# Kernel tuning notes

Hardware: AMD Instinct MI355X
Metric: run time of the kernel (lower is better)

Reference implementation:

```python
import jax, jax.numpy as jnp
import numpy as np

B, L, DIM, H, D = 4, 1024, 1024, 8, 32


def setup_inputs() -> dict:
    key = jax.random.key(0)
    ks = jax.random.split(key, 8)
    s = 0.02
    return dict(
        x=jax.random.normal(ks[0], (B, L, DIM), jnp.float32),
        W_in=jax.random.normal(ks[1], (DIM, DIM), jnp.float32) * s,
        b_in=jnp.zeros((DIM,), jnp.float32),
        W_qkva=jax.random.normal(ks[2], (H * D * 8, DIM), jnp.float32) * s,
        b_qkva=jnp.zeros((H * D * 8,), jnp.float32),
        W_y=jax.random.normal(ks[3], (DIM, H * D * 2), jnp.float32) * s,
        b_y=jnp.zeros((DIM,), jnp.float32),
        W_out=jax.random.normal(ks[4], (DIM, DIM), jnp.float32) * s,
        b_out=jnp.zeros((DIM,), jnp.float32),
        h0_re=jax.random.normal(ks[5], (H, D, D), jnp.float32),
        h0_im=jax.random.normal(ks[6], (H, D, D), jnp.float32),
    )


def reference(x, W_in, b_in, W_qkva, b_qkva, W_y, b_y, W_out, b_out, h0_re, h0_im):
    b, Ls, dim = x.shape
    Hh, Dd = h0_re.shape[0], h0_re.shape[1]
    u = jax.nn.silu(x @ W_in.T + b_in)
    qkva = (u @ W_qkva.T + b_qkva).reshape(b, Ls, Hh, Dd, 4, 2)
    c = jax.lax.complex(qkva[..., 0], qkva[..., 1])  # [b,L,H,D,4] complex
    q, k, v, a = c[..., 0], c[..., 1], c[..., 2], c[..., 3]
    mag2 = a.real * a.real + a.imag * a.imag
    # unit-modulus rotation scaled by sigmoid(log|a|^2) gate
    a = a * (jax.lax.rsqrt(mag2) * jax.nn.sigmoid(jnp.log(mag2)))
    kv = jnp.einsum('blhd,blhe->blhde', k, v)  # [b,L,H,D,D] complex
    h0 = jax.lax.complex(h0_re, h0_im)[None]  # [1,H,D,D]
    # fold initial state into step 0: h_0 = a_0 * h_init + kv_0
    kv = kv.at[:, 0].add(a[:, 0, ..., None] * h0)
    a_e = a[..., None]  # [b,L,H,D,1], broadcasts over state col dim

    def comb(c1, c2):
        a1, x1 = c1
        a2, x2 = c2
        return (a1 * a2, a2 * x1 + x2)

    # linear recurrence h_l = a_l * h_{l-1} + kv_l (equiv. to the FFT/cumsum
    # triangular-product matrix in the original module)
    _, h = jax.lax.associative_scan(comb, (a_e, kv), axis=1)
    y = jnp.einsum('blhd,blhde->blhe', q, h)  # [b,L,H,D] complex
    y2 = jnp.stack([y.real, y.imag], axis=-1).reshape(b, Ls, Hh * Dd * 2)
    y2 = jax.nn.silu(y2 @ W_y.T + b_y)
    return y2 @ W_out.T + b_out
```

## Files before the change

kernel.cpp:

```cpp
#include <hip/hip_runtime.h>

#define B_ 4
#define L_ 1024
#define DIM_ 1024
#define H_ 8
#define D_ 32
#define LSEG 32
#define NSEG (L_/LSEG)

typedef __bf16 bf16_t;
typedef __bf16 bf16x8 __attribute__((ext_vector_type(8)));
typedef float f32x4 __attribute__((ext_vector_type(4)));

__device__ __forceinline__ void gload_lds16(const bf16_t* g, bf16_t* l) {
  __builtin_amdgcn_global_load_lds((const __attribute__((address_space(1))) void*)g,
                                   (__attribute__((address_space(3))) void*)l, 16, 0, 0);
}
__device__ __forceinline__ void gload_lds16f(const float* g, float* l) {
  __builtin_amdgcn_global_load_lds((const __attribute__((address_space(1))) void*)g,
                                   (__attribute__((address_space(3))) void*)l, 16, 0, 0);
}

__global__ __launch_bounds__(256) void cvt_all(const float* __restrict__ x,
                                               const float* __restrict__ w1,
                                               const float* __restrict__ w2,
                                               const float* __restrict__ w3,
                                               const float* __restrict__ w4,
                                               bf16_t* __restrict__ ox,
                                               bf16_t* __restrict__ o1,
                                               bf16_t* __restrict__ o2,
                                               bf16_t* __restrict__ o3,
                                               bf16_t* __restrict__ o4) {
  int g = blockIdx.x;
  const float* in; bf16_t* out; int i;
  if      (g < 4096) { in = x;  out = ox; i = g * 256 + threadIdx.x; }
  else if (g < 5120) { in = w1; out = o1; i = (g - 4096) * 256 + threadIdx.x; }
  else if (g < 7168) { in = w2; out = o2; i = (g - 5120) * 256 + threadIdx.x; }
  else if (g < 7680) { in = w3; out = o3; i = (g - 7168) * 256 + threadIdx.x; }
  else               { in = w4; out = o4; i = (g - 7680) * 256 + threadIdx.x; }
  float4 v = ((const float4*)in)[i];
  union { bf16_t b[4]; unsigned long long q; } pk;
  pk.b[0] = (bf16_t)v.x; pk.b[1] = (bf16_t)v.y;
  pk.b[2] = (bf16_t)v.z; pk.b[3] = (bf16_t)v.w;
  ((unsigned long long*)out)[i] = pk.q;
}

template<int BN, int ACT, int OUTBF, int GATE>
__global__ __launch_bounds__(256) void gemm_nt(const bf16_t* __restrict__ A,
                                               const bf16_t* __restrict__ Bm,
                                               const float* __restrict__ bias,
                                               void* __restrict__ Cout,
                                               int M, int N, int K) {
  constexpr int NI = BN / 32;
  constexpr int ISS_B = BN / 32;
  __shared__ __align__(16) bf16_t As[128 * 64];
  __shared__ __align__(16) bf16_t Bs[BN * 64];
  const int t = threadIdx.x;
  const int wid = t >> 6, lane = t & 63;
  const int wr = wid >> 1, wc = wid & 1;
  const int lr = lane & 15, lq = lane >> 4;
  const int bm = blockIdx.x, bn = blockIdx.y;
  const int rA = wid * 32 + (lane >> 3);
  const int rB = wid * (BN / 4) + (lane >> 3);
  const int c8 = (((lane & 7) ^ ((lane >> 3) & 7))) * 8;
  const bf16_t* Ag = A + (size_t)(bm * 128 + rA) * K + c8;
  const bf16_t* Bg = Bm + (size_t)(bn * BN + rB) * K + c8;
  bf16_t* AsW = As + (wid * 32) * 64;
  bf16_t* BsW = Bs + (wid * (BN / 4)) * 64;
  f32x4 acc[4][NI] = {};
  for (int k0 = 0; k0 < K; k0 += 64) {
#pragma unroll
    for (int j = 0; j < 4; ++j)
      gload_lds16(Ag + (size_t)j * 8 * K, AsW + j * 8 * 64);
#pragma unroll
    for (int j = 0; j < ISS_B; ++j)
      gload_lds16(Bg + (size_t)j * 8 * K, BsW + j * 8 * 64);
    Ag += 64; Bg += 64;
    __syncthreads();
#pragma unroll
    for (int ks = 0; ks < 2; ++ks) {
      const int sg = ks * 4 + lq;
      const int sl = (sg ^ (lr & 7)) * 8;
      bf16x8 af[4], bfv[NI];
#pragma unroll
      for (int mi = 0; mi < 4; ++mi)
        af[mi] = *(const bf16x8*)&As[(wr * 64 + mi * 16 + lr) * 64 + sl];
#pragma unroll
      for (int ni = 0; ni < NI; ++ni)
        bfv[ni] = *(const bf16x8*)&Bs[(wc * (BN/2) + ni * 16 + lr) * 64 + sl];
#pragma unroll
      for (int mi = 0; mi < 4; ++mi)
#pragma unroll
        for (int ni = 0; ni < NI; ++ni)
          acc[mi][ni] = __builtin_amdgcn_mfma_f32_16x16x32_bf16(af[mi], bfv[ni], acc[mi][ni], 0, 0, 0);
    }
    __syncthreads();
  }
#pragma unroll
  for (int mi = 0; mi < 4; ++mi) {
#pragma unroll
    for (int ni = 0; ni < NI; ++ni) {
      int colg = bn * BN + wc * (BN/2) + ni * 16 + lr;
      float bb = bias[colg];
#pragma unroll
      for (int r = 0; r < 4; ++r) {
        int rowg = bm * 128 + wr * 64 + mi * 16 + lq * 4 + r;
        float v = acc[mi][ni][r] + bb;
        if (ACT == 1) v = v / (1.0f + __expf(-v));
        if (GATE) {
          float wv = __shfl_xor(v, 1);
          if ((colg & 7) >= 6) {
            float m2 = v * v + wv * wv;
            v *= sqrtf(m2) / (1.0f + m2);
          }
        }
        if (OUTBF) ((bf16_t*)Cout)[(size_t)rowg * N + colg] = (bf16_t)v;
        else       ((float*)Cout)[(size_t)rowg * N + colg] = v;
      }
    }
  }
}

template<int ACT, int OUTBF>
__global__ __launch_bounds__(256) void gemm64k(const bf16_t* __restrict__ A,
                                               const bf16_t* __restrict__ Bm,
                                               const float* __restrict__ bias,
                                               void* __restrict__ Cout,
                                               int M, int N, int K) {
  __shared__ __align__(16) bf16_t As[64 * 128];
  __shared__ __align__(16) bf16_t Bs[64 * 128];
  const int t = threadIdx.x;
  const int wid = t >> 6, lane = t & 63;
  const int wr = wid >> 1, wc = wid & 1;
  const int lr = lane & 15, lq = lane >> 4;
  const int bm = blockIdx.x, bn = blockIdx.y;
  const int crow = wid * 4 + (lane >> 4);
  const int c8 = ((lane & 15) ^ crow) * 8;
  const bf16_t* Ag = A + (size_t)(bm * 64 + crow) * K + c8;
  const bf16_t* Bg = Bm + (size_t)(bn * 64 + crow) * K + c8;
  bf16_t* AsW = As + (wid * 4) * 128;
  bf16_t* BsW = Bs + (wid * 4) * 128;
  f32x4 acc[2][2] = {};
  for (int k0 = 0; k0 < K; k0 += 128) {
#pragma unroll
    for (int j = 0; j < 4; ++j)
      gload_lds16(Ag + (size_t)j * 16 * K, AsW + j * 16 * 128);
#pragma unroll
    for (int j = 0; j < 4; ++j)
      gload_lds16(Bg + (size_t)j * 16 * K, BsW + j * 16 * 128);
    Ag += 128; Bg += 128;
    __syncthreads();
#pragma unroll
    for (int ks = 0; ks < 4; ++ks) {
      const int sg = ks * 4 + lq;
      const int sl = (sg ^ lr) * 8;
      bf16x8 af[2], bfv[2];
#pragma unroll
      for (int mi = 0; mi < 2; ++mi)
        af[mi] = *(const bf16x8*)&As[(wr * 32 + mi * 16 + lr) * 128 + sl];
#pragma unroll
      for (int ni = 0; ni < 2; ++ni)
        bfv[ni] = *(const bf16x8*)&Bs[(wc * 32 + ni * 16 + lr) * 128 + sl];
#pragma unroll
      for (int mi = 0; mi < 2; ++mi)
#pragma unroll
        for (int ni = 0; ni < 2; ++ni)
          acc[mi][ni] = __builtin_amdgcn_mfma_f32_16x16x32_bf16(af[mi], bfv[ni], acc[mi][ni], 0, 0, 0);
    }
    __syncthreads();
  }
#pragma unroll
  for (int mi = 0; mi < 2; ++mi) {
#pragma unroll
    for (int ni = 0; ni < 2; ++ni) {
      int colg = bn * 64 + wc * 32 + ni * 16 + lr;
      float bb = bias[colg];
#pragma unroll
      for (int r = 0; r < 4; ++r) {
        int rowg = bm * 64 + wr * 32 + mi * 16 + lq * 4 + r;
        float v = acc[mi][ni][r] + bb;
        if (ACT == 1) v = v / (1.0f + __expf(-v));
        if (OUTBF) ((bf16_t*)Cout)[(size_t)rowg * N + colg] = (bf16_t)v;
        else       ((float*)Cout)[(size_t)rowg * N + colg] = v;
      }
    }
  }
}

__global__ __launch_bounds__(256) void scan_seg(const float* __restrict__ qkva,
                                                float* __restrict__ y_loc,
                                                float* __restrict__ qP,
                                                float* __restrict__ Aseg,
                                                float* __restrict__ Hfin) {
  __shared__ __align__(16) float Q[LSEG * 256];
  const int t = threadIdx.x;
  const int seg = blockIdx.x;
  const int s = seg & (NSEG - 1);
  const int bh = seg >> 5;
  const int h = bh & (H_ - 1), b = bh >> 3;
  const int wid = t >> 6, lane = t & 63;
  const int dg = lane & 7, eh = lane >> 3;
  const int e = wid * 8 + eh;
  const float* gb = qkva + ((size_t)(b * L_ + s * LSEG) * H_ + h) * 256;
#pragma unroll
  for (int j = 0; j < 8; ++j) {
    const int l = wid * 8 + j;
    gload_lds16f(gb + (size_t)l * (H_ * 256) + lane * 4, Q + l * 256);
  }
  __syncthreads();
  float hr[4] = {}, hi[4] = {};
  float Pr[4] = {1,1,1,1}, Pi[4] = {0,0,0,0};
  const size_t row0 = ((size_t)(b * L_ + s * LSEG) * H_ + h) * D_;

  float4 qkA[4], qkB[4];
  float2 aaA[4], aaB[4];
  float2 vvA, vvB;

  auto LOADR = [&](int l, float4 (&qk)[4], float2 (&aa)[4], float2& vv) {
    const float* R = Q + l * 256;
    vv = *(const float2*)(R + e * 8 + 4);
#pragma unroll
    for (int j = 0; j < 4; ++j) {
      qk[j] = *(const float4*)(R + (dg + 8 * j) * 8);
      aa[j] = *(const float2*)(R + (dg + 8 * j) * 8 + 6);
    }
  };

  auto STEP = [&](int l, float4 (&qk)[4], float2 (&aa)[4], float2& vv) {
    const size_t rowl = row0 + (size_t)l * (H_ * D_);
    float ytr = 0.f, yti = 0.f;
    if (wid == 0) {
      float2 qpv[4];
#pragma unroll
      for (int j = 0; j < 4; ++j) {
        float nPr = aa[j].x * Pr[j] - aa[j].y * Pi[j];
        float nPi = aa[j].x * Pi[j] + aa[j].y * Pr[j];
        Pr[j] = nPr; Pi[j] = nPi;
        qpv[j].x = qk[j].x * nPr - qk[j].y * nPi;
        qpv[j].y = qk[j].x * nPi + qk[j].y * nPr;
      }
      if (lane < 8) {
#pragma unroll
        for (int j = 0; j < 4; ++j)
          *(float2*)(qP + (rowl + dg + 8 * j) * 2) = qpv[j];
      }
    }
#pragma unroll
    for (int j = 0; j < 4; ++j) {
      float kvr = qk[j].z * vv.x - qk[j].w * vv.y;
      float kvi = qk[j].z * vv.y + qk[j].w * vv.x;
      float nhr = aa[j].x * hr[j] - aa[j].y * hi[j] + kvr;
      float nhi = aa[j].x * hi[j] + aa[j].y * hr[j] + kvi;
      hr[j] = nhr; hi[j] = nhi;
      ytr += qk[j].x * nhr - qk[j].y * nhi;
      yti += qk[j].x * nhi + qk[j].y * nhr;
    }
    ytr += __shfl_down(ytr, 4); yti += __shfl_down(yti, 4);
    ytr += __shfl_down(ytr, 2); yti += __shfl_down(yti, 2);
    ytr += __shfl_down(ytr, 1); yti += __shfl_down(yti, 1);
    if (dg == 0)
      *(float2*)(y_loc + (rowl + e) * 2) = make_float2(ytr, yti);
  };

  LOADR(0, qkA, aaA, vvA);
  for (int l = 0; l < LSEG; l += 2) {
    LOADR(l + 1, qkB, aaB, vvB);
    STEP(l, qkA, aaA, vvA);
    LOADR(l + 2 < LSEG ? l + 2 : LSEG - 1, qkA, aaA, vvA);
    STEP(l + 1, qkB, aaB, vvB);
  }

  const size_t segb = (size_t)seg * D_;
  if (t < 8) {
#pragma unroll
    for (int j = 0; j < 4; ++j)
      *(float2*)(Aseg + (segb + dg + 8 * j) * 2) = make_float2(Pr[j], Pi[j]);
  }
#pragma unroll
  for (int j = 0; j < 4; ++j)
    *(float2*)(Hfin + ((segb + dg + 8 * j) * D_ + e) * 2) = make_float2(hr[j], hi[j]);
}

__global__ __launch_bounds__(128) void seg_combine(const float* __restrict__ h0re,
                                                   const float* __restrict__ h0im,
                                                   const float* __restrict__ Aseg,
                                                   const float* __restrict__ Hfin,
                                                   float* __restrict__ Hc) {
  const int bh = blockIdx.x >> 3;
  const int eg = blockIdx.x & 7;
  const int h = bh & (H_ - 1);
  const int t = threadIdx.x;
  const int d = t >> 2;
  const int e = eg * 4 + (t & 3);
  float cr = h0re[((size_t)h * D_ + d) * D_ + e];
  float ci = h0im[((size_t)h * D_ + d) * D_ + e];
  const size_t idx0  = ((size_t)bh * NSEG * D_ + d) * D_ + e;
  const size_t aidx0 = (size_t)bh * NSEG * D_ + d;
  float2 Ab[8], Fb[8];
#pragma unroll
  for (int p = 0; p < 8; ++p) {
    Ab[p] = *(const float2*)(Aseg + (aidx0 + (size_t)p * D_) * 2);
    Fb[p] = *(const float2*)(Hfin + (idx0 + (size_t)p * D_ * D_) * 2);
  }
  for (int so = 0; so < NSEG; so += 8) {
#pragma unroll
    for (int p = 0; p < 8; ++p) {
      const int s = so + p;
      float2 A0 = Ab[p], F0 = Fb[p];
      if (so + 8 < NSEG) {
        Ab[p] = *(const float2*)(Aseg + (aidx0 + (size_t)(s + 8) * D_) * 2);
        Fb[p] = *(const float2*)(Hfin + (idx0 + (size_t)(s + 8) * D_ * D_) * 2);
      }
      *(float2*)(Hc + (idx0 + (size_t)s * D_ * D_) * 2) = make_float2(cr, ci);
      float nr = A0.x * cr - A0.y * ci + F0.x;
      float ni = A0.x * ci + A0.y * cr + F0.y;
      cr = nr; ci = ni;
    }
  }
}

__global__ __launch_bounds__(256) void y_correct(const float* __restrict__ y_loc,
                                                 const float* __restrict__ qP,
                                                 const float* __restrict__ Hc,
                                                 bf16_t* __restrict__ y2b) {
  __shared__ __align__(16) float Hs[D_ * D_ * 2];
  const int seg = blockIdx.x;
  const int s = seg & (NSEG - 1);
  const int bh = seg >> 5;
  const int h = bh & (H_ - 1), b = bh >> 3;
  const int t = threadIdx.x;
  const float4* src = (const float4*)(Hc + (size_t)seg * (D_ * D_ * 2));
  ((float4*)Hs)[t] = src[t];
  ((float4*)Hs)[t + 256] = src[t + 256];
  __syncthreads();
  const int ep = (t & 15) * 2;
#pragma unroll
  for (int half = 0; half < 2; ++half) {
    const int l = half * 16 + (t >> 4);
    const int lg = s * LSEG + l;
    const size_t rowc = ((size_t)(b * L_ + lg) * H_ + h) * D_;
    const float* qpr = qP + rowc * 2;
    float4 y0 = *(const float4*)(y_loc + (rowc + ep) * 2);
    float ac_r[2] = {y0.x, y0.z}, ac_i[2] = {y0.y, y0.w};
#pragma unroll 4
    for (int d = 0; d < D_; ++d) {
      float2 p = *(const float2*)(qpr + d * 2);
      float4 hv = *(const float4*)&Hs[(d * D_ + ep) * 2];
      ac_r[0] += p.x * hv.x - p.y * hv.y; ac_i[0] += p.x * hv.y + p.y * hv.x;
      ac_r[1] += p.x * hv.z - p.y * hv.w; ac_i[1] += p.x * hv.w + p.y * hv.z;
    }
    union { bf16_t bv[4]; uint2 q; } pk;
    pk.bv[0] = (bf16_t)ac_r[0]; pk.bv[1] = (bf16_t)ac_i[0];
    pk.bv[2] = (bf16_t)ac_r[1]; pk.bv[3] = (bf16_t)ac_i[1];
    *(uint2*)(y2b + (size_t)(b * L_ + lg) * (H_ * D_ * 2) + (h * D_ + ep) * 2) = pk.q;
  }
}

extern "C" void kernel_launch(void* const* d_in, const int* in_sizes, int n_in,
                              void* d_out, int out_size, void* d_ws, size_t ws_size,
                              hipStream_t stream) {
  const float* x      = (const float*)d_in[0];
  const float* W_in   = (const float*)d_in[1];
  const float* b_in   = (const float*)d_in[2];
  const float* W_qkva = (const float*)d_in[3];
  const float* b_qkva = (const float*)d_in[4];
  const float* W_y    = (const float*)d_in[5];
  const float* b_y    = (const float*)d_in[6];
  const float* W_out  = (const float*)d_in[7];
  const float* b_out  = (const float*)d_in[8];
  const float* h0re   = (const float*)d_in[9];
  const float* h0im   = (const float*)d_in[10];

  char* w = (char*)d_ws;
  const size_t MB = 1ull << 20;
  bf16_t* Wb_in   = (bf16_t*)(w + 0*MB);
  bf16_t* Wb_qkva = (bf16_t*)(w + 2*MB);
  bf16_t* Wb_y    = (bf16_t*)(w + 6*MB);
  bf16_t* Wb_out  = (bf16_t*)(w + 7*MB);
  bf16_t* xb      = (bf16_t*)(w + 9*MB);
  float*  qP      = (float*) (w + 9*MB);
  bf16_t* u       = (bf16_t*)(w + 17*MB);
  float*  y_loc   = (float*) (w + 17*MB);
  float*  qkva    = (float*) (w + 25*MB);
  float*  Hc      = (float*) (w + 25*MB);
  bf16_t* y2b     = (bf16_t*)(w + 41*MB);
  bf16_t* z       = (bf16_t*)(w + 45*MB);
  float*  Aseg    = (float*) (w + 57*MB);
  float*  Hfin    = (float*) (w + 58*MB);

  cvt_all<<<8704, 256, 0, stream>>>(x, W_in, W_qkva, W_y, W_out,
                                    xb, Wb_in, Wb_qkva, Wb_y, Wb_out);

  gemm64k<1,1><<<dim3(64, 16), 256, 0, stream>>>(xb, Wb_in, b_in, u, 4096, 1024, 1024);
  gemm_nt<64,0,0,1><<<dim3(32, 32), 256, 0, stream>>>(u, Wb_qkva, b_qkva, qkva, 4096, 2048, 1024);
  scan_seg   <<<1024, 256, 0, stream>>>(qkva, y_loc, qP, Aseg, Hfin);
  seg_combine<<<256,  128, 0, stream>>>(h0re, h0im, Aseg, Hfin, Hc);
  y_correct  <<<1024, 256, 0, stream>>>(y_loc, qP, Hc, y2b);
  gemm64k<1,1><<<dim3(64, 16), 256, 0, stream>>>(y2b, Wb_y, b_y, z, 4096, 1024, 512);
  gemm64k<0,0><<<dim3(64, 16), 256, 0, stream>>>(z, Wb_out, b_out, (float*)d_out, 4096, 1024, 1024);
}
```

Measured before the change: 222.7 us.

## Enlarge GEMM tiles to 128x64 and parallelize scan prefix products across warps

The three 64x64 GEMMs become 128x64-tile GEMMs with half the grid, so each B tile is reused across twice as many rows and each warp runs more MFMAs per LDS load. In the segment scan, the cumulative decay product and the qP output are no longer computed serially by warp 0 inside the main recurrence loop. Each warp now computes a local product over its 8 rows, the partial products are combined through shared memory, and then qP is written. This takes work off the critical serial loop, at the cost of an extra barrier and a smaller grid (512 blocks) for the GEMMs, which may reduce occupancy on a 256-CU device.

```diff
diff --git a/kernel.cpp b/kernel.cpp
--- a/kernel.cpp
+++ b/kernel.cpp
@@ -122,12 +122,12 @@
 }
 
 template<int ACT, int OUTBF>
-__global__ __launch_bounds__(256) void gemm64k(const bf16_t* __restrict__ A,
-                                               const bf16_t* __restrict__ Bm,
-                                               const float* __restrict__ bias,
-                                               void* __restrict__ Cout,
-                                               int M, int N, int K) {
-  __shared__ __align__(16) bf16_t As[64 * 128];
+__global__ __launch_bounds__(256) void gemm_nt64(const bf16_t* __restrict__ A,
+                                                 const bf16_t* __restrict__ Bm,
+                                                 const float* __restrict__ bias,
+                                                 void* __restrict__ Cout,
+                                                 int M, int N, int K) {
+  __shared__ __align__(16) bf16_t As[128 * 128];
   __shared__ __align__(16) bf16_t Bs[64 * 128];
   const int t = threadIdx.x;
   const int wid = t >> 6, lane = t & 63;
@@ -136,14 +136,14 @@
   const int bm = blockIdx.x, bn = blockIdx.y;
   const int crow = wid * 4 + (lane >> 4);
   const int c8 = ((lane & 15) ^ crow) * 8;
-  const bf16_t* Ag = A + (size_t)(bm * 64 + crow) * K + c8;
+  const bf16_t* Ag = A + (size_t)(bm * 128 + crow) * K + c8;
   const bf16_t* Bg = Bm + (size_t)(bn * 64 + crow) * K + c8;
   bf16_t* AsW = As + (wid * 4) * 128;
   bf16_t* BsW = Bs + (wid * 4) * 128;
-  f32x4 acc[2][2] = {};
+  f32x4 acc[4][2] = {};
   for (int k0 = 0; k0 < K; k0 += 128) {
 #pragma unroll
-    for (int j = 0; j < 4; ++j)
+    for (int j = 0; j < 8; ++j)
       gload_lds16(Ag + (size_t)j * 16 * K, AsW + j * 16 * 128);
 #pragma unroll
     for (int j = 0; j < 4; ++j)
@@ -154,15 +154,15 @@
     for (int ks = 0; ks < 4; ++ks) {
       const int sg = ks * 4 + lq;
       const int sl = (sg ^ lr) * 8;
-      bf16x8 af[2], bfv[2];
-#pragma unroll
-      for (int mi = 0; mi < 2; ++mi)
-        af[mi] = *(const bf16x8*)&As[(wr * 32 + mi * 16 + lr) * 128 + sl];
+      bf16x8 af[4], bfv[2];
+#pragma unroll
+      for (int mi = 0; mi < 4; ++mi)
+        af[mi] = *(const bf16x8*)&As[(wr * 64 + mi * 16 + lr) * 128 + sl];
 #pragma unroll
       for (int ni = 0; ni < 2; ++ni)
         bfv[ni] = *(const bf16x8*)&Bs[(wc * 32 + ni * 16 + lr) * 128 + sl];
 #pragma unroll
-      for (int mi = 0; mi < 2; ++mi)
+      for (int mi = 0; mi < 4; ++mi)
 #pragma unroll
         for (int ni = 0; ni < 2; ++ni)
           acc[mi][ni] = __builtin_amdgcn_mfma_f32_16x16x32_bf16(af[mi], bfv[ni], acc[mi][ni], 0, 0, 0);
@@ -170,14 +170,14 @@
     __syncthreads();
   }
 #pragma unroll
-  for (int mi = 0; mi < 2; ++mi) {
+  for (int mi = 0; mi < 4; ++mi) {
 #pragma unroll
     for (int ni = 0; ni < 2; ++ni) {
       int colg = bn * 64 + wc * 32 + ni * 16 + lr;
       float bb = bias[colg];
 #pragma unroll
       for (int r = 0; r < 4; ++r) {
-        int rowg = bm * 64 + wr * 32 + mi * 16 + lq * 4 + r;
+        int rowg = bm * 128 + wr * 64 + mi * 16 + lq * 4 + r;
         float v = acc[mi][ni][r] + bb;
         if (ACT == 1) v = v / (1.0f + __expf(-v));
         if (OUTBF) ((bf16_t*)Cout)[(size_t)rowg * N + colg] = (bf16_t)v;
@@ -193,6 +193,7 @@
                                                 float* __restrict__ Aseg,
                                                 float* __restrict__ Hfin) {
   __shared__ __align__(16) float Q[LSEG * 256];
+  __shared__ __align__(16) float PP[4][D_ * 2];
   const int t = threadIdx.x;
   const int seg = blockIdx.x;
   const int s = seg & (NSEG - 1);
@@ -208,10 +209,64 @@
     gload_lds16f(gb + (size_t)l * (H_ * 256) + lane * 4, Q + l * 256);
   }
   __syncthreads();
+
+  const size_t row0 = ((size_t)(b * L_ + s * LSEG) * H_ + h) * D_;
+  const size_t segb = (size_t)seg * D_;
+  const int lb = wid * 8;
+
+  if (lane < 8) {
+    float2 LP[4] = {{1,0},{1,0},{1,0},{1,0}};
+    for (int l = lb; l < lb + 8; ++l) {
+      const float* R = Q + l * 256;
+#pragma unroll
+      for (int j = 0; j < 4; ++j) {
+        float2 aa = *(const float2*)(R + (dg + 8 * j) * 8 + 6);
+        float nr = aa.x * LP[j].x - aa.y * LP[j].y;
+        float ni = aa.x * LP[j].y + aa.y * LP[j].x;
+        LP[j].x = nr; LP[j].y = ni;
+      }
+    }
+#pragma unroll
+    for (int j = 0; j < 4; ++j)
+      *(float2*)&PP[wid][(dg + 8 * j) * 2] = LP[j];
+  }
+  __syncthreads();
+  if (lane < 8) {
+    float2 P[4] = {{1,0},{1,0},{1,0},{1,0}};
+    for (int w2 = 0; w2 < wid; ++w2) {
+#pragma unroll
+      for (int j = 0; j < 4; ++j) {
+        float2 lp = *(const float2*)&PP[w2][(dg + 8 * j) * 2];
+        float nr = lp.x * P[j].x - lp.y * P[j].y;
+        float ni = lp.x * P[j].y + lp.y * P[j].x;
+        P[j].x = nr; P[j].y = ni;
+      }
+    }
+    for (int l = lb; l < lb + 8; ++l) {
+      const float* R = Q + l * 256;
+      const size_t rowl = row0 + (size_t)l * (H_ * D_);
+#pragma unroll
+      for (int j = 0; j < 4; ++j) {
+        const int d = dg + 8 * j;
+        float2 aa = *(const float2*)(R + d * 8 + 6);
+        float nr = aa.x * P[j].x - aa.y * P[j].y;
+        float ni = aa.x * P[j].y + aa.y * P[j].x;
+        P[j].x = nr; P[j].y = ni;
+        float2 q = *(const float2*)(R + d * 8);
+        float2 qp;
+        qp.x = q.x * nr - q.y * ni;
+        qp.y = q.x * ni + q.y * nr;
+        *(float2*)(qP + (rowl + d) * 2) = qp;
+      }
+    }
+    if (wid == 3) {
+#pragma unroll
+      for (int j = 0; j < 4; ++j)
+        *(float2*)(Aseg + (segb + dg + 8 * j) * 2) = P[j];
+    }
+  }
+
   float hr[4] = {}, hi[4] = {};
-  float Pr[4] = {1,1,1,1}, Pi[4] = {0,0,0,0};
-  const size_t row0 = ((size_t)(b * L_ + s * LSEG) * H_ + h) * D_;
-
   float4 qkA[4], qkB[4];
   float2 aaA[4], aaB[4];
   float2 vvA, vvB;
@@ -229,22 +284,6 @@
   auto STEP = [&](int l, float4 (&qk)[4], float2 (&aa)[4], float2& vv) {
     const size_t rowl = row0 + (size_t)l * (H_ * D_);
     float ytr = 0.f, yti = 0.f;
-    if (wid == 0) {
-      float2 qpv[4];
-#pragma unroll
-      for (int j = 0; j < 4; ++j) {
-        float nPr = aa[j].x * Pr[j] - aa[j].y * Pi[j];
-        float nPi = aa[j].x * Pi[j] + aa[j].y * Pr[j];
-        Pr[j] = nPr; Pi[j] = nPi;
-        qpv[j].x = qk[j].x * nPr - qk[j].y * nPi;
-        qpv[j].y = qk[j].x * nPi + qk[j].y * nPr;
-      }
-      if (lane < 8) {
-#pragma unroll
-        for (int j = 0; j < 4; ++j)
-          *(float2*)(qP + (rowl + dg + 8 * j) * 2) = qpv[j];
-      }
-    }
 #pragma unroll
     for (int j = 0; j < 4; ++j) {
       float kvr = qk[j].z * vv.x - qk[j].w * vv.y;
@@ -270,12 +309,6 @@
     STEP(l + 1, qkB, aaB, vvB);
   }
 
-  const size_t segb = (size_t)seg * D_;
-  if (t < 8) {
-#pragma unroll
-    for (int j = 0; j < 4; ++j)
-      *(float2*)(Aseg + (segb + dg + 8 * j) * 2) = make_float2(Pr[j], Pi[j]);
-  }
 #pragma unroll
   for (int j = 0; j < 4; ++j)
     *(float2*)(Hfin + ((segb + dg + 8 * j) * D_ + e) * 2) = make_float2(hr[j], hi[j]);
@@ -391,11 +424,11 @@
   cvt_all<<<8704, 256, 0, stream>>>(x, W_in, W_qkva, W_y, W_out,
                                     xb, Wb_in, Wb_qkva, Wb_y, Wb_out);
 
-  gemm64k<1,1><<<dim3(64, 16), 256, 0, stream>>>(xb, Wb_in, b_in, u, 4096, 1024, 1024);
+  gemm_nt64<1,1><<<dim3(32, 16), 256, 0, stream>>>(xb, Wb_in, b_in, u, 4096, 1024, 1024);
   gemm_nt<64,0,0,1><<<dim3(32, 32), 256, 0, stream>>>(u, Wb_qkva, b_qkva, qkva, 4096, 2048, 1024);
   scan_seg   <<<1024, 256, 0, stream>>>(qkva, y_loc, qP, Aseg, Hfin);
   seg_combine<<<256,  128, 0, stream>>>(h0re, h0im, Aseg, Hfin, Hc);
   y_correct  <<<1024, 256, 0, stream>>>(y_loc, qP, Hc, y2b);
-  gemm64k<1,1><<<dim3(64, 16), 256, 0, stream>>>(y2b, Wb_y, b_y, z, 4096, 1024, 512);
-  gemm64k<0,0><<<dim3(64, 16), 256, 0, stream>>>(z, Wb_out, b_out, (float*)d_out, 4096, 1024, 1024);
-}
+  gemm_nt64<1,1><<<dim3(32, 16), 256, 0, stream>>>(y2b, Wb_y, b_y, z, 4096, 1024, 512);
+  gemm_nt64<0,0><<<dim3(32, 16), 256, 0, stream>>>(z, Wb_out, b_out, (float*)d_out, 4096, 1024, 1024);
+}
```

After: 222.9 us. About the same (+0.1%).

## Use 128x64 tiles with split-K and separate reduce for 1024x1024 GEMMs

Applied to the files above, without the earlier changes.

Replaces the 64x64-tile GEMM with a 128x64 tile for the W_y projection. The K=1024 projections (W_in, W_out) now use a split-K kernel that writes two fp32 partial results, followed by a reduce kernel that applies bias and activation. The larger tile improves operand reuse per block, and split-K keeps the grid at 1024 blocks. The cost is two extra kernel launches plus 32 MB of fp32 partial traffic per split-K GEMM, which could cancel out the gains.

```diff
diff --git a/kernel.cpp b/kernel.cpp
--- a/kernel.cpp
+++ b/kernel.cpp
@@ -122,12 +122,12 @@
 }
 
 template<int ACT, int OUTBF>
-__global__ __launch_bounds__(256) void gemm64k(const bf16_t* __restrict__ A,
-                                               const bf16_t* __restrict__ Bm,
-                                               const float* __restrict__ bias,
-                                               void* __restrict__ Cout,
-                                               int M, int N, int K) {
-  __shared__ __align__(16) bf16_t As[64 * 128];
+__global__ __launch_bounds__(256) void gemm_nt64(const bf16_t* __restrict__ A,
+                                                 const bf16_t* __restrict__ Bm,
+                                                 const float* __restrict__ bias,
+                                                 void* __restrict__ Cout,
+                                                 int M, int N, int K) {
+  __shared__ __align__(16) bf16_t As[128 * 128];
   __shared__ __align__(16) bf16_t Bs[64 * 128];
   const int t = threadIdx.x;
   const int wid = t >> 6, lane = t & 63;
@@ -136,14 +136,14 @@
   const int bm = blockIdx.x, bn = blockIdx.y;
   const int crow = wid * 4 + (lane >> 4);
   const int c8 = ((lane & 15) ^ crow) * 8;
-  const bf16_t* Ag = A + (size_t)(bm * 64 + crow) * K + c8;
+  const bf16_t* Ag = A + (size_t)(bm * 128 + crow) * K + c8;
   const bf16_t* Bg = Bm + (size_t)(bn * 64 + crow) * K + c8;
   bf16_t* AsW = As + (wid * 4) * 128;
   bf16_t* BsW = Bs + (wid * 4) * 128;
-  f32x4 acc[2][2] = {};
+  f32x4 acc[4][2] = {};
   for (int k0 = 0; k0 < K; k0 += 128) {
 #pragma unroll
-    for (int j = 0; j < 4; ++j)
+    for (int j = 0; j < 8; ++j)
       gload_lds16(Ag + (size_t)j * 16 * K, AsW + j * 16 * 128);
 #pragma unroll
     for (int j = 0; j < 4; ++j)
@@ -154,15 +154,15 @@
     for (int ks = 0; ks < 4; ++ks) {
       const int sg = ks * 4 + lq;
       const int sl = (sg ^ lr) * 8;
-      bf16x8 af[2], bfv[2];
-#pragma unroll
-      for (int mi = 0; mi < 2; ++mi)
-        af[mi] = *(const bf16x8*)&As[(wr * 32 + mi * 16 + lr) * 128 + sl];
+      bf16x8 af[4], bfv[2];
+#pragma unroll
+      for (int mi = 0; mi < 4; ++mi)
+        af[mi] = *(const bf16x8*)&As[(wr * 64 + mi * 16 + lr) * 128 + sl];
 #pragma unroll
       for (int ni = 0; ni < 2; ++ni)
         bfv[ni] = *(const bf16x8*)&Bs[(wc * 32 + ni * 16 + lr) * 128 + sl];
 #pragma unroll
-      for (int mi = 0; mi < 2; ++mi)
+      for (int mi = 0; mi < 4; ++mi)
 #pragma unroll
         for (int ni = 0; ni < 2; ++ni)
           acc[mi][ni] = __builtin_amdgcn_mfma_f32_16x16x32_bf16(af[mi], bfv[ni], acc[mi][ni], 0, 0, 0);
@@ -170,20 +170,109 @@
     __syncthreads();
   }
 #pragma unroll
-  for (int mi = 0; mi < 2; ++mi) {
+  for (int mi = 0; mi < 4; ++mi) {
 #pragma unroll
     for (int ni = 0; ni < 2; ++ni) {
       int colg = bn * 64 + wc * 32 + ni * 16 + lr;
       float bb = bias[colg];
 #pragma unroll
       for (int r = 0; r < 4; ++r) {
-        int rowg = bm * 64 + wr * 32 + mi * 16 + lq * 4 + r;
+        int rowg = bm * 128 + wr * 64 + mi * 16 + lq * 4 + r;
         float v = acc[mi][ni][r] + bb;
         if (ACT == 1) v = v / (1.0f + __expf(-v));
         if (OUTBF) ((bf16_t*)Cout)[(size_t)rowg * N + colg] = (bf16_t)v;
         else       ((float*)Cout)[(size_t)rowg * N + colg] = v;
       }
     }
+  }
+}
+
+__global__ __launch_bounds__(256) void gemm_splitk(const bf16_t* __restrict__ A,
+                                                   const bf16_t* __restrict__ Bm,
+                                                   float* __restrict__ Cpart,
+                                                   int M, int N, int K) {
+  __shared__ __align__(16) bf16_t As[128 * 64];
+  __shared__ __align__(16) bf16_t Bs[64 * 64];
+  const int t = threadIdx.x;
+  const int wid = t >> 6, lane = t & 63;
+  const int wr = wid >> 1, wc = wid & 1;
+  const int lr = lane & 15, lq = lane >> 4;
+  const int bm = blockIdx.x, bn = blockIdx.y, kh = blockIdx.z;
+  const int Kh = K >> 1;
+  const int rA = wid * 32 + (lane >> 3);
+  const int rB = wid * 16 + (lane >> 3);
+  const int c8 = (((lane & 7) ^ ((lane >> 3) & 7))) * 8;
+  const bf16_t* Ag = A + (size_t)(bm * 128 + rA) * K + kh * Kh + c8;
+  const bf16_t* Bg = Bm + (size_t)(bn * 64 + rB) * K + kh * Kh + c8;
+  bf16_t* AsW = As + (wid * 32) * 64;
+  bf16_t* BsW = Bs + (wid * 16) * 64;
+  f32x4 acc[4][2] = {};
+  for (int k0 = 0; k0 < Kh; k0 += 64) {
+#pragma unroll
+    for (int j = 0; j < 4; ++j)
+      gload_lds16(Ag + (size_t)j * 8 * K, AsW + j * 8 * 64);
+#pragma unroll
+    for (int j = 0; j < 2; ++j)
+      gload_lds16(Bg + (size_t)j * 8 * K, BsW + j * 8 * 64);
+    Ag += 64; Bg += 64;
+    __syncthreads();
+#pragma unroll
+    for (int ks = 0; ks < 2; ++ks) {
+      const int sg = ks * 4 + lq;
+      const int sl = (sg ^ (lr & 7)) * 8;
+      bf16x8 af[4], bfv[2];
+#pragma unroll
+      for (int mi = 0; mi < 4; ++mi)
+        af[mi] = *(const bf16x8*)&As[(wr * 64 + mi * 16 + lr) * 64 + sl];
+#pragma unroll
+      for (int ni = 0; ni < 2; ++ni)
+        bfv[ni] = *(const bf16x8*)&Bs[(wc * 32 + ni * 16 + lr) * 64 + sl];
+#pragma unroll
+      for (int mi = 0; mi < 4; ++mi)
+#pragma unroll
+        for (int ni = 0; ni < 2; ++ni)
+          acc[mi][ni] = __builtin_amdgcn_mfma_f32_16x16x32_bf16(af[mi], bfv[ni], acc[mi][ni], 0, 0, 0);
+    }
+    __syncthreads();
+  }
+  float* Cp = Cpart + (size_t)kh * M * N;
+#pragma unroll
+  for (int mi = 0; mi < 4; ++mi) {
+#pragma unroll
+    for (int ni = 0; ni < 2; ++ni) {
+      int colg = bn * 64 + wc * 32 + ni * 16 + lr;
+#pragma unroll
+      for (int r = 0; r < 4; ++r) {
+        int rowg = bm * 128 + wr * 64 + mi * 16 + lq * 4 + r;
+        Cp[(size_t)rowg * N + colg] = acc[mi][ni][r];
+      }
+    }
+  }
+}
+
+template<int ACT, int OUTBF>
+__global__ __launch_bounds__(256) void reduce_add(const float* __restrict__ p0,
+                                                  const float* __restrict__ p1,
+                                                  const float* __restrict__ bias,
+                                                  void* __restrict__ out, int N) {
+  const int i = blockIdx.x * 256 + threadIdx.x;
+  float4 a = ((const float4*)p0)[i];
+  float4 b = ((const float4*)p1)[i];
+  const int col = (i & (N / 4 - 1)) * 4;
+  float4 bb = *(const float4*)(bias + col);
+  float v[4] = {a.x + b.x + bb.x, a.y + b.y + bb.y,
+                a.z + b.z + bb.z, a.w + b.w + bb.w};
+  if (ACT) {
+#pragma unroll
+    for (int j = 0; j < 4; ++j) v[j] = v[j] / (1.0f + __expf(-v[j]));
+  }
+  if (OUTBF) {
+    union { bf16_t bq[4]; unsigned long long q; } pk;
+#pragma unroll
+    for (int j = 0; j < 4; ++j) pk.bq[j] = (bf16_t)v[j];
+    ((unsigned long long*)out)[i] = pk.q;
+  } else {
+    ((float4*)out)[i] = make_float4(v[0], v[1], v[2], v[3]);
   }
 }
 
@@ -387,15 +476,18 @@
   bf16_t* z       = (bf16_t*)(w + 45*MB);
   float*  Aseg    = (float*) (w + 57*MB);
   float*  Hfin    = (float*) (w + 58*MB);
+  float*  Pk      = (float*) (w + 66*MB);
 
   cvt_all<<<8704, 256, 0, stream>>>(x, W_in, W_qkva, W_y, W_out,
                                     xb, Wb_in, Wb_qkva, Wb_y, Wb_out);
 
-  gemm64k<1,1><<<dim3(64, 16), 256, 0, stream>>>(xb, Wb_in, b_in, u, 4096, 1024, 1024);
+  gemm_splitk<<<dim3(32, 16, 2), 256, 0, stream>>>(xb, Wb_in, Pk, 4096, 1024, 1024);
+  reduce_add<1,1><<<4096, 256, 0, stream>>>(Pk, Pk + 4096ull*1024, b_in, u, 1024);
   gemm_nt<64,0,0,1><<<dim3(32, 32), 256, 0, stream>>>(u, Wb_qkva, b_qkva, qkva, 4096, 2048, 1024);
   scan_seg   <<<1024, 256, 0, stream>>>(qkva, y_loc, qP, Aseg, Hfin);
   seg_combine<<<256,  128, 0, stream>>>(h0re, h0im, Aseg, Hfin, Hc);
   y_correct  <<<1024, 256, 0, stream>>>(y_loc, qP, Hc, y2b);
-  gemm64k<1,1><<<dim3(64, 16), 256, 0, stream>>>(y2b, Wb_y, b_y, z, 4096, 1024, 512);
-  gemm64k<0,0><<<dim3(64, 16), 256, 0, stream>>>(z, Wb_out, b_out, (float*)d_out, 4096, 1024, 1024);
-}
+  gemm_nt64<1,1><<<dim3(32, 16), 256, 0, stream>>>(y2b, Wb_y, b_y, z, 4096, 1024, 512);
+  gemm_splitk<<<dim3(32, 16, 2), 256, 0, stream>>>(z, Wb_out, Pk, 4096, 1024, 1024);
+  reduce_add<0,0><<<4096, 256, 0, stream>>>(Pk, Pk + 4096ull*1024, b_out, (float*)d_out, 1024);
+}
```

Result: slower. 234.1 us (+5.1%).
